# Kernel tuning notes

Hardware: AMD Instinct MI355X
Metric: run time of the kernel (lower is better)

## Reference

```python
import math
import jax, jax.numpy as jnp
import numpy as np

NQ = 10      # n_qubits
NB = 4       # n_blocks (angle encoding layers)
VD = 6       # vqc_depth (hardware-efficient layers)
LAT = 128    # latent_dim
NOBS = 9     # n_qubits - k_local + 1 sliding 2-local groups
DIM = 2 ** NQ


def sin_embed(t, dim):
    half = dim // 2
    freqs = jnp.exp(-math.log(10000.0) * jnp.arange(half, dtype=jnp.float32) / half)
    args = t[:, None] * freqs[None, :]
    return jnp.concatenate([jnp.cos(args), jnp.sin(args)], axis=-1)


def apply_ry(psi, theta, q):
    # psi: [B, 2^NQ] complex; theta: scalar or [B]
    B = psi.shape[0]
    p = psi.reshape(B, 2 ** q, 2, 2 ** (NQ - 1 - q))
    th = jnp.broadcast_to(theta, (B,))
    c = jnp.cos(th / 2)[:, None, None].astype(psi.dtype)
    s = jnp.sin(th / 2)[:, None, None].astype(psi.dtype)
    p0, p1 = p[:, :, 0, :], p[:, :, 1, :]
    return jnp.stack([c * p0 - s * p1, s * p0 + c * p1], axis=2).reshape(B, -1)


def apply_cnot(psi, ctrl, tgt):
    B = psi.shape[0]
    pt = psi.reshape((B,) + (2,) * NQ)
    p0 = jax.lax.index_in_dim(pt, 0, axis=ctrl + 1, keepdims=True)
    p1 = jnp.flip(jax.lax.index_in_dim(pt, 1, axis=ctrl + 1, keepdims=True), axis=tgt + 1)
    return jnp.concatenate([p0, p1], axis=ctrl + 1).reshape(B, -1)


def run_circuit(enc, var_params):
    B = enc.shape[0]
    psi = jnp.zeros((B, DIM), dtype=jnp.complex64).at[:, 0].set(1.0)
    # angle encoding: RY data re-uploading blocks with CNOT ladders between blocks
    for layer in range(NB):
        for q in range(NQ):
            psi = apply_ry(psi, enc[:, layer * NQ + q], q)
        if layer < NB - 1:
            for q in range(0, NQ - 1, 2):
                psi = apply_cnot(psi, q, q + 1)
            for q in range(1, NQ - 1, 2):
                psi = apply_cnot(psi, q, q + 1)
    # hardware-efficient variational layers
    for ly in range(VD):
        for q in range(NQ):
            psi = apply_ry(psi, var_params[ly, q], q)
        for q in range(0, NQ - 1, 2):
            psi = apply_cnot(psi, q, q + 1)
        for q in range(1, NQ - 1, 2):
            psi = apply_cnot(psi, q, q + 1)
    return psi


def build_H(A_p, B_p, D_p):
    # create_Hermitian: lower-tri (row-major) = A + iB; h[i-1,i-1] = D[i]; H = h + h^dagger
    r, c = np.tril_indices(4, -1)  # order matches count+j loop: (1,0),(2,0),(2,1),(3,0),(3,1),(3,2)
    L = jnp.zeros((NOBS, 4, 4), dtype=jnp.complex64)
    L = L.at[:, r, c].set(A_p.astype(jnp.complex64) + 1j * B_p.astype(jnp.complex64))
    d = 2.0 * jnp.concatenate([D_p[:, 1:4], jnp.zeros((NOBS, 1), dtype=D_p.dtype)], axis=1)
    H = L + jnp.conj(jnp.swapaxes(L, 1, 2))
    H = H + jax.vmap(jnp.diag)(d).astype(jnp.complex64)
    return H


def expvals(psi, H):
    B = psi.shape[0]
    outs = []
    for s in range(NOBS):  # sliding window [s, s+1]
        pg = psi.reshape(B, 2 ** s, 4, 2 ** (NQ - s - 2))
        outs.append(jnp.einsum('balr,lk,bakr->b', jnp.conj(pg), H[s], pg).real)
    return jnp.stack(outs, axis=-1)


def setup_inputs() -> dict:
    ks = jax.random.split(jax.random.key(0), 12)
    B = 2048
    return {
        'z_t': jax.random.normal(ks[0], (B, LAT), dtype=jnp.float32),
        't': jax.random.uniform(ks[1], (B,), dtype=jnp.float32),
        'W1': 0.05 * jax.random.normal(ks[2], (2 * LAT, 256), dtype=jnp.float32),
        'b1': jnp.zeros((256,), dtype=jnp.float32),
        'W2': 0.05 * jax.random.normal(ks[3], (256, NB * NQ), dtype=jnp.float32),
        'b2': jnp.zeros((NB * NQ,), dtype=jnp.float32),
        'var_params': 0.01 * jax.random.normal(ks[4], (VD, NQ), dtype=jnp.float32),
        'A_p': 2.0 * jax.random.normal(ks[5], (NOBS, 6), dtype=jnp.float32),
        'B_p': 2.0 * jax.random.normal(ks[6], (NOBS, 6), dtype=jnp.float32),
        'D_p': 2.0 * jax.random.normal(ks[7], (NOBS, 4), dtype=jnp.float32),
        'W3': 0.05 * jax.random.normal(ks[8], (NOBS, 256), dtype=jnp.float32),
        'b3': jnp.zeros((256,), dtype=jnp.float32),
        'W4': 0.05 * jax.random.normal(ks[9], (256, LAT), dtype=jnp.float32),
        'b4': jnp.zeros((LAT,), dtype=jnp.float32),
    }


def reference(z_t, t, W1, b1, W2, b2, var_params, A_p, B_p, D_p, W3, b3, W4, b4):
    x = jnp.concatenate([z_t, sin_embed(t, LAT)], axis=-1)   # [B, 2*LAT]
    h = jax.nn.silu(x @ W1 + b1)
    enc = h @ W2 + b2                                         # [B, NB*NQ]
    psi = run_circuit(enc, var_params)                        # [B, 2^NQ]
    obs = expvals(psi, build_H(A_p, B_p, D_p))                # [B, NOBS]
    return jax.nn.silu(obs @ W3 + b3) @ W4 + b4               # [B, LAT]
```

## Files before the change

### kernel.cpp

```cpp
#include <hip/hip_runtime.h>
#include <math.h>

#define NOBS 9
#define LATD 128

typedef unsigned u32x2 __attribute__((ext_vector_type(2)));

__device__ __forceinline__ float silu_f(float x) { return x / (1.f + expf(-x)); }


template<int CTRL>
__device__ __forceinline__ float dpp_perm(float x) {
  return __int_as_float(__builtin_amdgcn_update_dpp(0, __float_as_int(x), CTRL, 0xF, 0xF, true));
}
template<int PAT>
__device__ __forceinline__ float ds_swz(float x) {
  return __int_as_float(__builtin_amdgcn_ds_swizzle(__float_as_int(x), PAT));
}

__device__ __forceinline__ float x4(float x) { return ds_swz<0x101F>(x); }

#if __has_builtin(__builtin_amdgcn_permlane32_swap)
#define PL32 1
__device__ __forceinline__ float x32(float x, bool sel) {
  u32x2 r = __builtin_amdgcn_permlane32_swap(__float_as_uint(x), __float_as_uint(x), false, false);
  return __uint_as_float(sel ? r.x : r.y);
}
__device__ __forceinline__ float sum32(float x) {
  u32x2 r = __builtin_amdgcn_permlane32_swap(__float_as_uint(x), __float_as_uint(x), false, false);
  return __uint_as_float(r.x) + __uint_as_float(r.y);
}
#else
#define PL32 0
__device__ __forceinline__ float x32(float x, bool sel) { return __shfl_xor(x, 32, 64); }
__device__ __forceinline__ float sum32(float x) { return x + __shfl_xor(x, 32, 64); }
#endif

#if __has_builtin(__builtin_amdgcn_permlane16_swap)
#define PL16 1
__device__ __forceinline__ float x16(float x, bool sel) {
  u32x2 r = __builtin_amdgcn_permlane16_swap(__float_as_uint(x), __float_as_uint(x), false, false);
  return __uint_as_float(sel ? r.x : r.y);
}
__device__ __forceinline__ float sum16(float x) {
  u32x2 r = __builtin_amdgcn_permlane16_swap(__float_as_uint(x), __float_as_uint(x), false, false);
  return __uint_as_float(r.x) + __uint_as_float(r.y);
}
#else
#define PL16 0
__device__ __forceinline__ float x16(float x, bool sel) { return ds_swz<0x401F>(x); }
__device__ __forceinline__ float sum16(float x) { return x + ds_swz<0x401F>(x); }
#endif

__device__ __forceinline__ float wave_sum(float x) {
  x += dpp_perm<0xB1>(x);
  x += dpp_perm<0x4E>(x);
  x += x4(x);
  x += dpp_perm<0x128>(x);
  x = sum16(x);
  x = sum32(x);
  return x;
}


template<int M>
__device__ __forceinline__ void ry_reg(float v[16], float c, float s) {
#pragma unroll
  for (int r = 0; r < 16; ++r) {
    if ((r & M) == 0) {
      float p0 = v[r], p1 = v[r | M];
      v[r]     = c * p0 - s * p1;
      v[r | M] = s * p0 + c * p1;
    }
  }
}

__device__ __forceinline__ void apply_rys(float v[16], int lane, bool sel32, bool sel16,
                                          const float* __restrict__ cc,
                                          const float* __restrict__ ss) {
  ry_reg<8>(v, cc[0], ss[0]);
  ry_reg<4>(v, cc[1], ss[1]);
  ry_reg<2>(v, cc[2], ss[2]);
  ry_reg<1>(v, cc[3], ss[3]);
  { float c = cc[4], s = ss[4], sp = (lane & 32) ? s : -s;
#pragma unroll
    for (int r = 0; r < 16; ++r) { float p = x32(v[r], sel32); v[r] = fmaf(c, v[r], sp * p); } }
  { float c = cc[5], s = ss[5], sp = (lane & 16) ? s : -s;
#pragma unroll
    for (int r = 0; r < 16; ++r) { float p = x16(v[r], sel16); v[r] = fmaf(c, v[r], sp * p); } }
  { float c = cc[6], s = ss[6], sp = (lane & 8) ? s : -s;
#pragma unroll
    for (int r = 0; r < 16; ++r) { float p = dpp_perm<0x128>(v[r]); v[r] = fmaf(c, v[r], sp * p); } }
  { float c = cc[7], s = ss[7], sp = (lane & 4) ? s : -s;
#pragma unroll
    for (int r = 0; r < 16; ++r) { float p = x4(v[r]); v[r] = fmaf(c, v[r], sp * p); } }
  { float c = cc[8], s = ss[8], sp = (lane & 2) ? s : -s;
#pragma unroll
    for (int r = 0; r < 16; ++r) { float p = dpp_perm<0x4E>(v[r]); v[r] = fmaf(c, v[r], sp * p); } }
  { float c = cc[9], s = ss[9], sp = (lane & 1) ? s : -s;
#pragma unroll
    for (int r = 0; r < 16; ++r) { float p = dpp_perm<0xB1>(v[r]); v[r] = fmaf(c, v[r], sp * p); } }
}

__device__ __forceinline__ void cnot_ladder(float v[16], int lane, bool sel32, bool sel16) {
  float t;
  t=v[8];  v[8]=v[12];  v[12]=t;
  t=v[9];  v[9]=v[13];  v[13]=t;
  t=v[10]; v[10]=v[14]; v[14]=t;
  t=v[11]; v[11]=v[15]; v[15]=t;
  t=v[2];  v[2]=v[3];   v[3]=t;
  t=v[6];  v[6]=v[7];   v[7]=t;
  t=v[10]; v[10]=v[11]; v[11]=t;
  t=v[14]; v[14]=v[15]; v[15]=t;
  { bool c45 = (lane & 32);
#pragma unroll
    for (int r = 0; r < 16; ++r) { float p = x16(v[r], sel16); v[r] = c45 ? p : v[r]; } }
  { bool c67 = (lane & 8);
#pragma unroll
    for (int r = 0; r < 16; ++r) { float p = x4(v[r]); v[r] = c67 ? p : v[r]; } }
  { bool c89 = (lane & 2);
#pragma unroll
    for (int r = 0; r < 16; ++r) { float p = dpp_perm<0xB1>(v[r]); v[r] = c89 ? p : v[r]; } }
  t=v[4];  v[4]=v[6];   v[6]=t;
  t=v[5];  v[5]=v[7];   v[7]=t;
  t=v[12]; v[12]=v[14]; v[14]=t;
  t=v[13]; v[13]=v[15]; v[15]=t;
#pragma unroll
  for (int r = 1; r < 16; r += 2) v[r] = x32(v[r], sel32);
  { bool c56 = (lane & 16);
#pragma unroll
    for (int r = 0; r < 16; ++r) { float p = dpp_perm<0x128>(v[r]); v[r] = c56 ? p : v[r]; } }
  { bool c78 = (lane & 4);
#pragma unroll
    for (int r = 0; r < 16; ++r) { float p = dpp_perm<0x4E>(v[r]); v[r] = c78 ? p : v[r]; } }
}


__global__ __launch_bounds__(256) void fused_kernel(
    const float* __restrict__ z, const float* __restrict__ t,
    const float* __restrict__ W1, const float* __restrict__ b1,
    const float* __restrict__ W2, const float* __restrict__ b2,
    const float* __restrict__ varp,
    const float* __restrict__ A_p, const float* __restrict__ D_p,
    const float* __restrict__ W3, const float* __restrict__ b3,
    const float* __restrict__ W4, const float* __restrict__ b4,
    float* __restrict__ out) {
  __shared__ float xs[4][256];
  __shared__ float hs[4][256];
  __shared__ float dump[4][1024];
  __shared__ float cs[4][40], sn[4][40];
  __shared__ float vcs[60], vsn[60];
  __shared__ float os[4][NOBS];

  int tid = threadIdx.x;
  int b0 = blockIdx.x * 4;

  if (tid < 60) {
    float s, c;
    sincosf(0.5f * varp[tid], &s, &c);
    vcs[tid] = c; vsn[tid] = s;
  }

#pragma unroll
  for (int r = 0; r < 4; ++r) {
    int b = b0 + r;
    if (tid < 128) {
      xs[r][tid] = z[b * 128 + tid];
    } else {
      int i = tid - 128, j = i & 63;
      float freq = expf(-9.2103403719761836f * (float)j * (1.f / 64.f));
      float arg = t[b] * freq;
      xs[r][tid] = (i < 64) ? cosf(arg) : sinf(arg);
    }
  }
  __syncthreads();

  {
    float bv = b1[tid];
    float a0 = bv, a1 = bv, a2 = bv, a3 = bv;
#pragma unroll 4
    for (int k = 0; k < 256; k += 4) {
      float w0 = W1[(k + 0) * 256 + tid];
      float w1 = W1[(k + 1) * 256 + tid];
      float w2 = W1[(k + 2) * 256 + tid];
      float w3 = W1[(k + 3) * 256 + tid];
      float4 x0 = *(const float4*)&xs[0][k];
      float4 x1 = *(const float4*)&xs[1][k];
      float4 x2 = *(const float4*)&xs[2][k];
      float4 x3 = *(const float4*)&xs[3][k];
      a0 = fmaf(x0.w, w3, fmaf(x0.z, w2, fmaf(x0.y, w1, fmaf(x0.x, w0, a0))));
      a1 = fmaf(x1.w, w3, fmaf(x1.z, w2, fmaf(x1.y, w1, fmaf(x1.x, w0, a1))));
      a2 = fmaf(x2.w, w3, fmaf(x2.z, w2, fmaf(x2.y, w1, fmaf(x2.x, w0, a2))));
      a3 = fmaf(x3.w, w3, fmaf(x3.z, w2, fmaf(x3.y, w1, fmaf(x3.x, w0, a3))));
    }
    hs[0][tid] = silu_f(a0);
    hs[1][tid] = silu_f(a1);
    hs[2][tid] = silu_f(a2);
    hs[3][tid] = silu_f(a3);
  }
  __syncthreads();

  if (tid < 160) {
    int r = tid / 40, c = tid - r * 40;
    float acc = b2[c];
#pragma unroll 4
    for (int k = 0; k < 256; k += 4) {
      float4 h = *(const float4*)&hs[r][k];
      acc = fmaf(h.x, W2[(k + 0) * 40 + c], acc);
      acc = fmaf(h.y, W2[(k + 1) * 40 + c], acc);
      acc = fmaf(h.z, W2[(k + 2) * 40 + c], acc);
      acc = fmaf(h.w, W2[(k + 3) * 40 + c], acc);
    }
    float s, cv;
    sincosf(0.5f * acc, &s, &cv);
    cs[r][c] = cv; sn[r][c] = s;
  }
  __syncthreads();

  {
    int wave = tid >> 6;
    int lane = tid & 63;
    bool sel32 = true, sel16 = true;
#if PL32
    { u32x2 tt = __builtin_amdgcn_permlane32_swap((unsigned)lane, (unsigned)lane, false, false);
      sel32 = (tt.x == (unsigned)(lane ^ 32)); }
#endif
#if PL16
    { u32x2 tt = __builtin_amdgcn_permlane16_swap((unsigned)lane, (unsigned)lane, false, false);
      sel16 = (tt.x == (unsigned)(lane ^ 16)); }
#endif
    const float* cc = cs[wave];
    const float* ss = sn[wave];

    float base = 1.f;
    base *= (lane & 32) ? ss[4] : cc[4];
    base *= (lane & 16) ? ss[5] : cc[5];
    base *= (lane & 8)  ? ss[6] : cc[6];
    base *= (lane & 4)  ? ss[7] : cc[7];
    base *= (lane & 2)  ? ss[8] : cc[8];
    base *= (lane & 1)  ? ss[9] : cc[9];
    float v[16];
#pragma unroll
    for (int r = 0; r < 16; ++r) {
      float p = base;
      p *= (r & 8) ? ss[0] : cc[0];
      p *= (r & 4) ? ss[1] : cc[1];
      p *= (r & 2) ? ss[2] : cc[2];
      p *= (r & 1) ? ss[3] : cc[3];
      v[r] = p;
    }
    cnot_ladder(v, lane, sel32, sel16);
#pragma unroll 1
    for (int layer = 1; layer < 4; ++layer) {
      apply_rys(v, lane, sel32, sel16, cc + layer * 10, ss + layer * 10);
      if (layer < 3) cnot_ladder(v, lane, sel32, sel16);
    }
#pragma unroll 1
    for (int ly = 0; ly < 6; ++ly) {
      apply_rys(v, lane, sel32, sel16, vcs + ly * 10, vsn + ly * 10);
      cnot_ladder(v, lane, sel32, sel16);
    }

    float* sw = dump[wave];
#pragma unroll
    for (int r = 0; r < 16; ++r) sw[r * 64 + lane] = v[r];

#pragma unroll 1
    for (int s = 0; s < NOBS; ++s) {
      const int r8 = 8 - s;
      const int stride = 1 << r8;
      float h10 = A_p[s*6+0], h20 = A_p[s*6+1], h21 = A_p[s*6+2];
      float h30 = A_p[s*6+3], h31 = A_p[s*6+4], h32 = A_p[s*6+5];
      float d0 = 2.f * D_p[s*4+1], d1 = 2.f * D_p[s*4+2], d2 = 2.f * D_p[s*4+3];
      float acc = 0.f;
#pragma unroll
      for (int k = 0; k < 4; ++k) {
        int p = lane + 64 * k;
        int a  = p >> r8;
        int rr = p & (stride - 1);
        int bse = (a << (r8 + 2)) + rr;
        float x0 = sw[bse];
        float x1 = sw[bse + stride];
        float x2 = sw[bse + 2 * stride];
        float x3 = sw[bse + 3 * stride];
        acc += d0 * x0 * x0 + d1 * x1 * x1 + d2 * x2 * x2
             + 2.f * (h10 * x1 * x0 + h20 * x2 * x0 + h21 * x2 * x1
                    + h30 * x3 * x0 + h31 * x3 * x1 + h32 * x3 * x2);
      }
      acc = wave_sum(acc);
      if (lane == 0) os[wave][s] = acc;
    }
  }
  __syncthreads();

  {
    float bv = b3[tid];
    float a0 = bv, a1 = bv, a2 = bv, a3 = bv;
#pragma unroll
    for (int s = 0; s < NOBS; ++s) {
      float w = W3[s * 256 + tid];
      a0 = fmaf(os[0][s], w, a0);
      a1 = fmaf(os[1][s], w, a1);
      a2 = fmaf(os[2][s], w, a2);
      a3 = fmaf(os[3][s], w, a3);
    }
    hs[0][tid] = silu_f(a0);
    hs[1][tid] = silu_f(a1);
    hs[2][tid] = silu_f(a2);
    hs[3][tid] = silu_f(a3);
  }
  __syncthreads();
  {
    int c = tid & 127, rg = tid >> 7;
    const float* h0 = hs[rg * 2];
    const float* h1 = hs[rg * 2 + 1];
    float o0 = b4[c], o1 = b4[c];
#pragma unroll 4
    for (int k = 0; k < 256; k += 4) {
      float w0 = W4[(k + 0) * 128 + c];
      float w1 = W4[(k + 1) * 128 + c];
      float w2 = W4[(k + 2) * 128 + c];
      float w3 = W4[(k + 3) * 128 + c];
      float4 ha = *(const float4*)&h0[k];
      float4 hb = *(const float4*)&h1[k];
      o0 = fmaf(ha.w, w3, fmaf(ha.z, w2, fmaf(ha.y, w1, fmaf(ha.x, w0, o0))));
      o1 = fmaf(hb.w, w3, fmaf(hb.z, w2, fmaf(hb.y, w1, fmaf(hb.x, w0, o1))));
    }
    out[(b0 + rg * 2) * LATD + c]     = o0;
    out[(b0 + rg * 2 + 1) * LATD + c] = o1;
  }
}


extern "C" void kernel_launch(void* const* d_in, const int* in_sizes, int n_in,
                              void* d_out, int out_size, void* d_ws, size_t ws_size,
                              hipStream_t stream) {
  const float* z_t  = (const float*)d_in[0];
  const float* t    = (const float*)d_in[1];
  const float* W1   = (const float*)d_in[2];
  const float* b1   = (const float*)d_in[3];
  const float* W2   = (const float*)d_in[4];
  const float* b2   = (const float*)d_in[5];
  const float* varp = (const float*)d_in[6];
  const float* A_p  = (const float*)d_in[7];
  const float* D_p  = (const float*)d_in[9];
  const float* W3   = (const float*)d_in[10];
  const float* b3   = (const float*)d_in[11];
  const float* W4   = (const float*)d_in[12];
  const float* b4   = (const float*)d_in[13];
  float* out = (float*)d_out;

  int B = in_sizes[1];

  fused_kernel<<<B / 4, 256, 0, stream>>>(z_t, t, W1, b1, W2, b2, varp,
                                          A_p, D_p, W3, b3, W4, b4, out);
}
```

Measured before the change: 128.8 us.

## Use packed FMA with prefetched weights and shuffle-based CNOT permutations

Interleaves batch rows in shared memory as float2 pairs so the dense layers can issue packed two-wide FMAs. Weight loads are software-prefetched in chunks of 16 so global latency overlaps with the arithmetic. The three and three chained masked-swap stages in each CNOT ladder become single __shfl permutations per half. The permlane swap helpers are replaced by __shfl_xor and ds_swizzle. Using shfl, which goes through LDS bpermute, could cost more per exchange than the DPP and permlane paths it replaces, and the prefetch buffers raise register pressure.

```diff
diff --git a/kernel.cpp b/kernel.cpp
--- a/kernel.cpp
+++ b/kernel.cpp
@@ -4,9 +4,11 @@
 #define NOBS 9
 #define LATD 128
 
-typedef unsigned u32x2 __attribute__((ext_vector_type(2)));
+typedef float f2 __attribute__((ext_vector_type(2)));
 
 __device__ __forceinline__ float silu_f(float x) { return x / (1.f + expf(-x)); }
+__device__ __forceinline__ f2 splat2(float x) { return (f2){x, x}; }
+__device__ __forceinline__ f2 fma2(f2 a, f2 b, f2 c) { return __builtin_elementwise_fma(a, b, c); }
 
 
 template<int CTRL>
@@ -17,48 +19,15 @@
 __device__ __forceinline__ float ds_swz(float x) {
   return __int_as_float(__builtin_amdgcn_ds_swizzle(__float_as_int(x), PAT));
 }
-
-__device__ __forceinline__ float x4(float x) { return ds_swz<0x101F>(x); }
-
-#if __has_builtin(__builtin_amdgcn_permlane32_swap)
-#define PL32 1
-__device__ __forceinline__ float x32(float x, bool sel) {
-  u32x2 r = __builtin_amdgcn_permlane32_swap(__float_as_uint(x), __float_as_uint(x), false, false);
-  return __uint_as_float(sel ? r.x : r.y);
-}
-__device__ __forceinline__ float sum32(float x) {
-  u32x2 r = __builtin_amdgcn_permlane32_swap(__float_as_uint(x), __float_as_uint(x), false, false);
-  return __uint_as_float(r.x) + __uint_as_float(r.y);
-}
-#else
-#define PL32 0
-__device__ __forceinline__ float x32(float x, bool sel) { return __shfl_xor(x, 32, 64); }
-__device__ __forceinline__ float sum32(float x) { return x + __shfl_xor(x, 32, 64); }
-#endif
-
-#if __has_builtin(__builtin_amdgcn_permlane16_swap)
-#define PL16 1
-__device__ __forceinline__ float x16(float x, bool sel) {
-  u32x2 r = __builtin_amdgcn_permlane16_swap(__float_as_uint(x), __float_as_uint(x), false, false);
-  return __uint_as_float(sel ? r.x : r.y);
-}
-__device__ __forceinline__ float sum16(float x) {
-  u32x2 r = __builtin_amdgcn_permlane16_swap(__float_as_uint(x), __float_as_uint(x), false, false);
-  return __uint_as_float(r.x) + __uint_as_float(r.y);
-}
-#else
-#define PL16 0
-__device__ __forceinline__ float x16(float x, bool sel) { return ds_swz<0x401F>(x); }
-__device__ __forceinline__ float sum16(float x) { return x + ds_swz<0x401F>(x); }
-#endif
+__device__ __forceinline__ float x4f(float x) { return ds_swz<0x101F>(x); }
 
 __device__ __forceinline__ float wave_sum(float x) {
   x += dpp_perm<0xB1>(x);
   x += dpp_perm<0x4E>(x);
-  x += x4(x);
+  x += x4f(x);
   x += dpp_perm<0x128>(x);
-  x = sum16(x);
-  x = sum32(x);
+  x += ds_swz<0x401F>(x);
+  x += __shfl_xor(x, 32, 64);
   return x;
 }
 
@@ -75,7 +44,7 @@
   }
 }
 
-__device__ __forceinline__ void apply_rys(float v[16], int lane, bool sel32, bool sel16,
+__device__ __forceinline__ void apply_rys(float v[16], int lane,
                                           const float* __restrict__ cc,
                                           const float* __restrict__ ss) {
   ry_reg<8>(v, cc[0], ss[0]);
@@ -84,16 +53,16 @@
   ry_reg<1>(v, cc[3], ss[3]);
   { float c = cc[4], s = ss[4], sp = (lane & 32) ? s : -s;
 #pragma unroll
-    for (int r = 0; r < 16; ++r) { float p = x32(v[r], sel32); v[r] = fmaf(c, v[r], sp * p); } }
+    for (int r = 0; r < 16; ++r) { float p = __shfl_xor(v[r], 32, 64); v[r] = fmaf(c, v[r], sp * p); } }
   { float c = cc[5], s = ss[5], sp = (lane & 16) ? s : -s;
 #pragma unroll
-    for (int r = 0; r < 16; ++r) { float p = x16(v[r], sel16); v[r] = fmaf(c, v[r], sp * p); } }
+    for (int r = 0; r < 16; ++r) { float p = __shfl_xor(v[r], 16, 64); v[r] = fmaf(c, v[r], sp * p); } }
   { float c = cc[6], s = ss[6], sp = (lane & 8) ? s : -s;
 #pragma unroll
     for (int r = 0; r < 16; ++r) { float p = dpp_perm<0x128>(v[r]); v[r] = fmaf(c, v[r], sp * p); } }
   { float c = cc[7], s = ss[7], sp = (lane & 4) ? s : -s;
 #pragma unroll
-    for (int r = 0; r < 16; ++r) { float p = x4(v[r]); v[r] = fmaf(c, v[r], sp * p); } }
+    for (int r = 0; r < 16; ++r) { float p = x4f(v[r]); v[r] = fmaf(c, v[r], sp * p); } }
   { float c = cc[8], s = ss[8], sp = (lane & 2) ? s : -s;
 #pragma unroll
     for (int r = 0; r < 16; ++r) { float p = dpp_perm<0x4E>(v[r]); v[r] = fmaf(c, v[r], sp * p); } }
@@ -102,7 +71,7 @@
     for (int r = 0; r < 16; ++r) { float p = dpp_perm<0xB1>(v[r]); v[r] = fmaf(c, v[r], sp * p); } }
 }
 
-__device__ __forceinline__ void cnot_ladder(float v[16], int lane, bool sel32, bool sel16) {
+__device__ __forceinline__ void cnot_ladder(float v[16], int lane) {
   float t;
   t=v[8];  v[8]=v[12];  v[12]=t;
   t=v[9];  v[9]=v[13];  v[13]=t;
@@ -112,27 +81,17 @@
   t=v[6];  v[6]=v[7];   v[7]=t;
   t=v[10]; v[10]=v[11]; v[11]=t;
   t=v[14]; v[14]=v[15]; v[15]=t;
-  { bool c45 = (lane & 32);
-#pragma unroll
-    for (int r = 0; r < 16; ++r) { float p = x16(v[r], sel16); v[r] = c45 ? p : v[r]; } }
-  { bool c67 = (lane & 8);
-#pragma unroll
-    for (int r = 0; r < 16; ++r) { float p = x4(v[r]); v[r] = c67 ? p : v[r]; } }
-  { bool c89 = (lane & 2);
-#pragma unroll
-    for (int r = 0; r < 16; ++r) { float p = dpp_perm<0xB1>(v[r]); v[r] = c89 ? p : v[r]; } }
+  int se = lane ^ ((lane & 42) >> 1);
+#pragma unroll
+  for (int r = 0; r < 16; ++r) v[r] = __shfl(v[r], se, 64);
   t=v[4];  v[4]=v[6];   v[6]=t;
   t=v[5];  v[5]=v[7];   v[7]=t;
   t=v[12]; v[12]=v[14]; v[14]=t;
   t=v[13]; v[13]=v[15]; v[15]=t;
-#pragma unroll
-  for (int r = 1; r < 16; r += 2) v[r] = x32(v[r], sel32);
-  { bool c56 = (lane & 16);
-#pragma unroll
-    for (int r = 0; r < 16; ++r) { float p = dpp_perm<0x128>(v[r]); v[r] = c56 ? p : v[r]; } }
-  { bool c78 = (lane & 4);
-#pragma unroll
-    for (int r = 0; r < 16; ++r) { float p = dpp_perm<0x4E>(v[r]); v[r] = c78 ? p : v[r]; } }
+  int so  = lane ^ ((lane & 20) >> 1);
+  int so1 = so ^ 32;
+#pragma unroll
+  for (int r = 0; r < 16; ++r) v[r] = __shfl(v[r], (r & 1) ? so1 : so, 64);
 }
 
 
@@ -145,8 +104,9 @@
     const float* __restrict__ W3, const float* __restrict__ b3,
     const float* __restrict__ W4, const float* __restrict__ b4,
     float* __restrict__ out) {
-  __shared__ float xs[4][256];
+  __shared__ f2    xsA[256], xsB[256];
   __shared__ float hs[4][256];
+  __shared__ f2    hp[2][256];
   __shared__ float dump[4][1024];
   __shared__ float cs[4][40], sn[4][40];
   __shared__ float vcs[60], vsn[60];
@@ -161,55 +121,69 @@
     vcs[tid] = c; vsn[tid] = s;
   }
 
-#pragma unroll
-  for (int r = 0; r < 4; ++r) {
-    int b = b0 + r;
-    if (tid < 128) {
-      xs[r][tid] = z[b * 128 + tid];
-    } else {
-      int i = tid - 128, j = i & 63;
-      float freq = expf(-9.2103403719761836f * (float)j * (1.f / 64.f));
-      float arg = t[b] * freq;
-      xs[r][tid] = (i < 64) ? cosf(arg) : sinf(arg);
+  if (tid < 128) {
+#pragma unroll
+    for (int r = 0; r < 4; ++r) {
+      float val = z[(b0 + r) * 128 + tid];
+      if (r < 2) ((float*)xsA)[2 * tid + r]       = val;
+      else       ((float*)xsB)[2 * tid + (r - 2)] = val;
+    }
+  } else {
+    int i = tid - 128, j = i & 63;
+    float freq = expf(-9.2103403719761836f * (float)j * (1.f / 64.f));
+#pragma unroll
+    for (int r = 0; r < 4; ++r) {
+      float arg = t[b0 + r] * freq;
+      float val = (i < 64) ? cosf(arg) : sinf(arg);
+      int k = 128 + i;
+      if (r < 2) ((float*)xsA)[2 * k + r]       = val;
+      else       ((float*)xsB)[2 * k + (r - 2)] = val;
     }
   }
   __syncthreads();
 
   {
-    float bv = b1[tid];
-    float a0 = bv, a1 = bv, a2 = bv, a3 = bv;
-#pragma unroll 4
-    for (int k = 0; k < 256; k += 4) {
-      float w0 = W1[(k + 0) * 256 + tid];
-      float w1 = W1[(k + 1) * 256 + tid];
-      float w2 = W1[(k + 2) * 256 + tid];
-      float w3 = W1[(k + 3) * 256 + tid];
-      float4 x0 = *(const float4*)&xs[0][k];
-      float4 x1 = *(const float4*)&xs[1][k];
-      float4 x2 = *(const float4*)&xs[2][k];
-      float4 x3 = *(const float4*)&xs[3][k];
-      a0 = fmaf(x0.w, w3, fmaf(x0.z, w2, fmaf(x0.y, w1, fmaf(x0.x, w0, a0))));
-      a1 = fmaf(x1.w, w3, fmaf(x1.z, w2, fmaf(x1.y, w1, fmaf(x1.x, w0, a1))));
-      a2 = fmaf(x2.w, w3, fmaf(x2.z, w2, fmaf(x2.y, w1, fmaf(x2.x, w0, a2))));
-      a3 = fmaf(x3.w, w3, fmaf(x3.z, w2, fmaf(x3.y, w1, fmaf(x3.x, w0, a3))));
-    }
-    hs[0][tid] = silu_f(a0);
-    hs[1][tid] = silu_f(a1);
-    hs[2][tid] = silu_f(a2);
-    hs[3][tid] = silu_f(a3);
+    f2 a01 = splat2(b1[tid]), a23 = a01;
+    float w[16];
+#pragma unroll
+    for (int j = 0; j < 16; ++j) w[j] = W1[j * 256 + tid];
+#pragma unroll 1
+    for (int k0 = 0; k0 < 256; k0 += 16) {
+      int kn = (k0 + 16) & 255;
+      float wn[16];
+#pragma unroll
+      for (int j = 0; j < 16; ++j) wn[j] = W1[(kn + j) * 256 + tid];
+#pragma unroll
+      for (int j = 0; j < 16; ++j) {
+        a01 = fma2(xsA[k0 + j], splat2(w[j]), a01);
+        a23 = fma2(xsB[k0 + j], splat2(w[j]), a23);
+      }
+#pragma unroll
+      for (int j = 0; j < 16; ++j) w[j] = wn[j];
+    }
+    hs[0][tid] = silu_f(a01.x);
+    hs[1][tid] = silu_f(a01.y);
+    hs[2][tid] = silu_f(a23.x);
+    hs[3][tid] = silu_f(a23.y);
   }
   __syncthreads();
 
   if (tid < 160) {
     int r = tid / 40, c = tid - r * 40;
     float acc = b2[c];
-#pragma unroll 4
-    for (int k = 0; k < 256; k += 4) {
-      float4 h = *(const float4*)&hs[r][k];
-      acc = fmaf(h.x, W2[(k + 0) * 40 + c], acc);
-      acc = fmaf(h.y, W2[(k + 1) * 40 + c], acc);
-      acc = fmaf(h.z, W2[(k + 2) * 40 + c], acc);
-      acc = fmaf(h.w, W2[(k + 3) * 40 + c], acc);
+    float w[16];
+#pragma unroll
+    for (int j = 0; j < 16; ++j) w[j] = W2[j * 40 + c];
+#pragma unroll 1
+    for (int k0 = 0; k0 < 256; k0 += 16) {
+      int kn = (k0 + 16) & 255;
+      float wn[16];
+#pragma unroll
+      for (int j = 0; j < 16; ++j) wn[j] = W2[(kn + j) * 40 + c];
+#pragma unroll
+      for (int j = 0; j < 16; ++j) acc = fmaf(hs[r][k0 + j], w[j], acc);
+#pragma unroll
+      for (int j = 0; j < 16; ++j) w[j] = wn[j];
     }
     float s, cv;
     sincosf(0.5f * acc, &s, &cv);
@@ -220,15 +194,6 @@
   {
     int wave = tid >> 6;
     int lane = tid & 63;
-    bool sel32 = true, sel16 = true;
-#if PL32
-    { u32x2 tt = __builtin_amdgcn_permlane32_swap((unsigned)lane, (unsigned)lane, false, false);
-      sel32 = (tt.x == (unsigned)(lane ^ 32)); }
-#endif
-#if PL16
-    { u32x2 tt = __builtin_amdgcn_permlane16_swap((unsigned)lane, (unsigned)lane, false, false);
-      sel16 = (tt.x == (unsigned)(lane ^ 16)); }
-#endif
     const float* cc = cs[wave];
     const float* ss = sn[wave];
 
@@ -249,16 +214,16 @@
       p *= (r & 1) ? ss[3] : cc[3];
       v[r] = p;
     }
-    cnot_ladder(v, lane, sel32, sel16);
+    cnot_ladder(v, lane);
 #pragma unroll 1
     for (int layer = 1; layer < 4; ++layer) {
-      apply_rys(v, lane, sel32, sel16, cc + layer * 10, ss + layer * 10);
-      if (layer < 3) cnot_ladder(v, lane, sel32, sel16);
+      apply_rys(v, lane, cc + layer * 10, ss + layer * 10);
+      if (layer < 3) cnot_ladder(v, lane);
     }
 #pragma unroll 1
     for (int ly = 0; ly < 6; ++ly) {
-      apply_rys(v, lane, sel32, sel16, vcs + ly * 10, vsn + ly * 10);
-      cnot_ladder(v, lane, sel32, sel16);
+      apply_rys(v, lane, vcs + ly * 10, vsn + ly * 10);
+      cnot_ladder(v, lane);
     }
 
     float* sw = dump[wave];
@@ -294,40 +259,38 @@
   __syncthreads();
 
   {
-    float bv = b3[tid];
-    float a0 = bv, a1 = bv, a2 = bv, a3 = bv;
+    f2 a01 = splat2(b3[tid]), a23 = a01;
 #pragma unroll
     for (int s = 0; s < NOBS; ++s) {
-      float w = W3[s * 256 + tid];
-      a0 = fmaf(os[0][s], w, a0);
-      a1 = fmaf(os[1][s], w, a1);
-      a2 = fmaf(os[2][s], w, a2);
-      a3 = fmaf(os[3][s], w, a3);
-    }
-    hs[0][tid] = silu_f(a0);
-    hs[1][tid] = silu_f(a1);
-    hs[2][tid] = silu_f(a2);
-    hs[3][tid] = silu_f(a3);
-  }
-  __syncthreads();
+      float wv = W3[s * 256 + tid];
+      a01 = fma2((f2){os[0][s], os[1][s]}, splat2(wv), a01);
+      a23 = fma2((f2){os[2][s], os[3][s]}, splat2(wv), a23);
+    }
+    hp[0][tid] = (f2){silu_f(a01.x), silu_f(a01.y)};
+    hp[1][tid] = (f2){silu_f(a23.x), silu_f(a23.y)};
+  }
+  __syncthreads();
+
   {
     int c = tid & 127, rg = tid >> 7;
-    const float* h0 = hs[rg * 2];
-    const float* h1 = hs[rg * 2 + 1];
-    float o0 = b4[c], o1 = b4[c];
-#pragma unroll 4
-    for (int k = 0; k < 256; k += 4) {
-      float w0 = W4[(k + 0) * 128 + c];
-      float w1 = W4[(k + 1) * 128 + c];
-      float w2 = W4[(k + 2) * 128 + c];
-      float w3 = W4[(k + 3) * 128 + c];
-      float4 ha = *(const float4*)&h0[k];
-      float4 hb = *(const float4*)&h1[k];
-      o0 = fmaf(ha.w, w3, fmaf(ha.z, w2, fmaf(ha.y, w1, fmaf(ha.x, w0, o0))));
-      o1 = fmaf(hb.w, w3, fmaf(hb.z, w2, fmaf(hb.y, w1, fmaf(hb.x, w0, o1))));
-    }
-    out[(b0 + rg * 2) * LATD + c]     = o0;
-    out[(b0 + rg * 2 + 1) * LATD + c] = o1;
+    const f2* hr = hp[rg];
+    f2 acc = splat2(b4[c]);
+    float w[16];
+#pragma unroll
+    for (int j = 0; j < 16; ++j) w[j] = W4[j * 128 + c];
+#pragma unroll 1
+    for (int k0 = 0; k0 < 256; k0 += 16) {
+      int kn = (k0 + 16) & 255;
+      float wn[16];
+#pragma unroll
+      for (int j = 0; j < 16; ++j) wn[j] = W4[(kn + j) * 128 + c];
+#pragma unroll
+      for (int j = 0; j < 16; ++j) acc = fma2(hr[k0 + j], splat2(w[j]), acc);
+#pragma unroll
+      for (int j = 0; j < 16; ++j) w[j] = wn[j];
+    }
+    out[(b0 + rg * 2) * LATD + c]     = acc.x;
+    out[(b0 + rg * 2 + 1) * LATD + c] = acc.y;
   }
 }
 
```

Result: faster. 124.2 us (-3.6%).
